# Optimization experiments

Hardware: AMD Instinct MI355X
Metric: run time of the kernel (lower is better)

Reference implementation:

```python
import jax, jax.numpy as jnp
import numpy as np


def setup_inputs() -> dict:
    key = jax.random.key(0)
    k1, k2, k3 = jax.random.split(key, 3)
    B, S, A, C = 128, 52, 5, 20
    predictions = jax.random.normal(k1, (B, A * (5 + C), S, S), dtype=jnp.float32)
    t = jax.random.uniform(k2, (B, S, S, A, 5 + C), dtype=jnp.float32)
    mask = (jax.random.uniform(k3, (B, S, S, A)) < 0.05).astype(jnp.float32)
    targets = t.at[..., 4].set(mask)
    anchors = jnp.array([[1.08, 1.19], [3.42, 4.41], [6.63, 11.38],
                         [9.42, 5.11], [16.62, 10.52]], dtype=jnp.float32)
    return {"predictions": predictions, "targets": targets, "anchors": anchors}


def _yolov2_loss(predictions, targets, anchors):
    B, pred_dim, S, _ = predictions.shape
    A = anchors.shape[0]
    C = pred_dim // A - 5
    # [B, A, 5+C, S, S] -> [B, S, S, A, 5+C]
    p = predictions.reshape(B, A, 5 + C, S, S).transpose(0, 3, 4, 1, 2)
    tx, ty, tw, th = p[..., 0], p[..., 1], p[..., 2], p[..., 3]
    conf_logits = p[..., 4]
    class_logits = p[..., 5:]

    gx, gy, gw, gh = targets[..., 0], targets[..., 1], targets[..., 2], targets[..., 3]
    obj_mask = targets[..., 4]
    class_target = targets[..., 5:]

    pred_cx = jax.nn.sigmoid(tx)
    pred_cy = jax.nn.sigmoid(ty)
    pred_w = jnp.exp(tw) * anchors[:, 0]  # broadcast over trailing A dim
    pred_h = jnp.exp(th) * anchors[:, 1]

    # grid offsets: dim 1 is i (row -> cy), dim 2 is j (col -> cx)
    jj = jnp.arange(S, dtype=jnp.float32)[None, None, :, None]
    ii = jnp.arange(S, dtype=jnp.float32)[None, :, None, None]
    cx_gt, cy_gt = gx + jj, gy + ii
    cx_pr, cy_pr = pred_cx + jj, pred_cy + ii

    # vectorized corner-form IoU (only used where obj_mask == 1)
    x1min, x1max = cx_gt - gw / 2, cx_gt + gw / 2
    y1min, y1max = cy_gt - gh / 2, cy_gt + gh / 2
    x2min, x2max = cx_pr - pred_w / 2, cx_pr + pred_w / 2
    y2min, y2max = cy_pr - pred_h / 2, cy_pr + pred_h / 2
    inter_w = jnp.clip(jnp.minimum(x1max, x2max) - jnp.maximum(x1min, x2min), 0.0)
    inter_h = jnp.clip(jnp.minimum(y1max, y2max) - jnp.maximum(y1min, y2min), 0.0)
    inter = inter_w * inter_h
    union = gw * gh + pred_w * pred_h - inter
    iou = jnp.where(union > 0, inter / union, 0.0)

    loss_xy = jnp.sum(obj_mask * (jnp.square(pred_cx - gx) + jnp.square(pred_cy - gy)))
    eps = 1e-6
    loss_wh = jnp.sum(obj_mask * (jnp.square(jnp.sqrt(pred_w + eps) - jnp.sqrt(gw + eps))
                                  + jnp.square(jnp.sqrt(pred_h + eps) - jnp.sqrt(gh + eps))))

    conf_pred = jax.nn.sigmoid(conf_logits)
    loss_obj = jnp.sum(obj_mask * jnp.square(iou - conf_pred))
    loss_noobj = jnp.sum((1.0 - obj_mask) * jnp.square(conf_pred))

    # BCE with logits: softplus(x) - x * t (stable via logaddexp)
    bce = jnp.logaddexp(0.0, class_logits) - class_logits * class_target
    loss_cls = jnp.sum(obj_mask[..., None] * bce)

    total = 5.0 * (loss_xy + loss_wh) + 5.0 * loss_obj + 0.5 * loss_noobj + loss_cls
    return total, loss_xy + loss_wh, loss_cls, loss_obj + loss_noobj


def reference(predictions, targets, anchors):
    # returns (total, coord, class, obj) matching the original dict values
    return _yolov2_loss(predictions, targets, anchors)
```

## Files before the change

kernel.cpp:

```cpp
#include <hip/hip_runtime.h>

#define S_DIM 52
#define SS 2704
#define NA 5
#define NC 20
#define NB 128
#define CELLS (NB * SS)
#define BLOCK 256
#define NBLK (CELLS / BLOCK)

__device__ __forceinline__ float fast_sigmoid(float x) {
    return __builtin_amdgcn_rcpf(1.0f + __expf(-x));
}
__device__ __forceinline__ float fast_softplus(float x) {
    return fmaxf(x, 0.0f) + __logf(1.0f + __expf(-fabsf(x)));
}

__device__ __forceinline__ bool block_reduce4(float v0, float v1, float v2, float v3,
                                              float a[4]) {
    #pragma unroll
    for (int off = 32; off > 0; off >>= 1) {
        v0 += __shfl_xor(v0, off, 64);
        v1 += __shfl_xor(v1, off, 64);
        v2 += __shfl_xor(v2, off, 64);
        v3 += __shfl_xor(v3, off, 64);
    }
    __shared__ float red[4][4];
    int wid = threadIdx.x >> 6, lane = threadIdx.x & 63;
    if (lane == 0) {
        red[wid][0] = v0; red[wid][1] = v1; red[wid][2] = v2; red[wid][3] = v3;
    }
    __syncthreads();
    if (threadIdx.x == 0) {
        #pragma unroll
        for (int q = 0; q < 4; ++q)
            a[q] = red[0][q] + red[1][q] + red[2][q] + red[3][q];
        return true;
    }
    return false;
}

__global__ __launch_bounds__(BLOCK) void yolo_main(
        const float* __restrict__ P,
        const float* __restrict__ T,
        const float* __restrict__ anch,
        float* __restrict__ partial) {
    int cell = blockIdx.x * BLOCK + threadIdx.x;
    int b  = cell / SS;
    int ij = cell - b * SS;
    const float* Pb = P + (size_t)b * 125 * SS + ij;
    const float* Tc = T + (size_t)cell * 125;

    float fl[NA], cf[NA];
    #pragma unroll
    for (int a = 0; a < NA; ++a) fl[a] = Tc[a * 25 + 4];
    #pragma unroll
    for (int a = 0; a < NA; ++a) cf[a] = Pb[(size_t)(a * 25 + 4) * SS];

    float s_xywh = 0.0f, s_cls = 0.0f, s_obj = 0.0f, s_noobj = 0.0f;

    #pragma unroll
    for (int a = 0; a < NA; ++a) {
        float cp = fast_sigmoid(cf[a]);
        if (fl[a] != 0.0f) {
            const float* Pa = Pb + (size_t)(a * 25) * SS;
            const float* Ta = Tc + a * 25;
            float aw = anch[2 * a], ahv = anch[2 * a + 1];

            float tx = Pa[0], ty = Pa[SS], tw = Pa[2 * SS], th = Pa[3 * SS];
            float gx = Ta[0], gy = Ta[1], gw = Ta[2], gh = Ta[3];
            float cx = fast_sigmoid(tx), cy = fast_sigmoid(ty);
            float pw = __expf(tw) * aw;
            float ph = __expf(th) * ahv;
            float iw = fmaxf(fminf(gx + 0.5f * gw, cx + 0.5f * pw) -
                             fmaxf(gx - 0.5f * gw, cx - 0.5f * pw), 0.0f);
            float ih = fmaxf(fminf(gy + 0.5f * gh, cy + 0.5f * ph) -
                             fmaxf(gy - 0.5f * gh, cy - 0.5f * ph), 0.0f);
            float inter = iw * ih;
            float uni   = gw * gh + pw * ph - inter;
            float iou   = (uni > 0.0f) ? inter * __builtin_amdgcn_rcpf(uni) : 0.0f;

            float dx = cx - gx, dy = cy - gy;
            s_xywh += dx * dx + dy * dy;
            const float eps = 1e-6f;
            float dw = __fsqrt_rn(pw + eps) - __fsqrt_rn(gw + eps);
            float dh = __fsqrt_rn(ph + eps) - __fsqrt_rn(gh + eps);
            s_xywh += dw * dw + dh * dh;

            float dob = iou - cp;
            s_obj += dob * dob;

            #pragma unroll
            for (int k = 0; k < NC; ++k) {
                float l = Pa[(size_t)(5 + k) * SS];
                float t = Ta[5 + k];
                s_cls += fast_softplus(l) - l * t;
            }
        } else {
            s_noobj += cp * cp;
        }
    }

    float a4[4];
    if (block_reduce4(s_xywh, s_cls, s_obj, s_noobj, a4)) {
        float* p = partial + (size_t)blockIdx.x * 4;
        p[0] = a4[0]; p[1] = a4[1]; p[2] = a4[2]; p[3] = a4[3];
    }
}

__global__ __launch_bounds__(BLOCK) void yolo_reduce(
        const float* __restrict__ partial, int n, float* __restrict__ out) {
    float v0 = 0.0f, v1 = 0.0f, v2 = 0.0f, v3 = 0.0f;
    for (int i = threadIdx.x; i < n; i += BLOCK) {
        const float* p = partial + (size_t)i * 4;
        v0 += p[0]; v1 += p[1]; v2 += p[2]; v3 += p[3];
    }
    float a4[4];
    if (block_reduce4(v0, v1, v2, v3, a4)) {
        float xywh = a4[0], cls = a4[1], obj = a4[2], noobj = a4[3];
        out[0] = 5.0f * xywh + 5.0f * obj + 0.5f * noobj + cls;
        out[1] = xywh;
        out[2] = cls;
        out[3] = obj + noobj;
    }
}

extern "C" void kernel_launch(void* const* d_in, const int* in_sizes, int n_in,
                              void* d_out, int out_size, void* d_ws, size_t ws_size,
                              hipStream_t stream) {
    const float* P = (const float*)d_in[0];
    const float* T = (const float*)d_in[1];
    const float* anch = (const float*)d_in[2];
    float* out = (float*)d_out;
    float* partial = (float*)d_ws;

    yolo_main<<<NBLK, BLOCK, 0, stream>>>(P, T, anch, partial);
    yolo_reduce<<<1, BLOCK, 0, stream>>>(partial, NBLK, out);
}
```

Measured before the change: 68.98 us.

## Stage target tile in LDS with coalesced float4 loads, one wave per anchor

Each block now handles 64 cells and copies their contiguous target rows (64×125 floats) into shared memory with coalesced float4 loads. Before, each thread read its own 125-float strided row. Each of the five waves then handles one anchor, so the per-anchor branch becomes per-thread rather than a loop inside each thread. The aim is to cut uncoalesced global reads of the target tensor. The cost is about 32KB of LDS per block, which may limit occupancy, plus an extra barrier. It also changes the number of partials sent to the reduce kernel.

```diff
diff --git a/kernel.cpp b/kernel.cpp
--- a/kernel.cpp
+++ b/kernel.cpp
@@ -1,13 +1,16 @@
 #include <hip/hip_runtime.h>
 
-#define S_DIM 52
 #define SS 2704
 #define NA 5
 #define NC 20
 #define NB 128
 #define CELLS (NB * SS)
-#define BLOCK 256
-#define NBLK (CELLS / BLOCK)
+#define TILE 64
+#define TPB 320
+#define NTILE (CELLS / TILE)
+#define TILE_F (TILE * 125)
+#define TILE_V4 (TILE_F / 4)
+#define RBLOCK 256
 
 __device__ __forceinline__ float fast_sigmoid(float x) {
     return __builtin_amdgcn_rcpf(1.0f + __expf(-x));
@@ -16,8 +19,104 @@
     return fmaxf(x, 0.0f) + __logf(1.0f + __expf(-fabsf(x)));
 }
 
-__device__ __forceinline__ bool block_reduce4(float v0, float v1, float v2, float v3,
-                                              float a[4]) {
+__global__ __launch_bounds__(TPB) void yolo_main(
+        const float* __restrict__ P,
+        const float* __restrict__ T,
+        const float* __restrict__ anch,
+        float* __restrict__ partial) {
+    __shared__ float lds[TILE_F];
+    __shared__ float red[NA][4];
+
+    int tile = blockIdx.x;
+
+    const float4* src = (const float4*)(T + (size_t)tile * TILE_F);
+    float4* dst = (float4*)lds;
+    #pragma unroll
+    for (int i = 0; i < 7; ++i) {
+        int idx = threadIdx.x + i * TPB;
+        if (idx < TILE_V4) dst[idx] = src[idx];
+    }
+    __syncthreads();
+
+    int a    = threadIdx.x >> 6;
+    int lane = threadIdx.x & 63;
+    int cell = tile * TILE + lane;
+    int b    = cell / SS;
+    int ij   = cell - b * SS;
+
+    const float* Pa = P + ((size_t)b * 125 + a * 25) * SS + ij;
+    const float* Tl = lds + lane * 125 + a * 25;
+    float aw  = anch[2 * a];
+    float ahv = anch[2 * a + 1];
+
+    float fl = Tl[4];
+    float cp = fast_sigmoid(Pa[4 * SS]);
+
+    float s_xywh = 0.0f, s_cls = 0.0f, s_obj = 0.0f, s_noobj = 0.0f;
+
+    if (fl != 0.0f) {
+        float tx = Pa[0], ty = Pa[SS], tw = Pa[2 * SS], th = Pa[3 * SS];
+        float gx = Tl[0], gy = Tl[1], gw = Tl[2], gh = Tl[3];
+        float cx = fast_sigmoid(tx), cy = fast_sigmoid(ty);
+        float pw = __expf(tw) * aw;
+        float ph = __expf(th) * ahv;
+        float iw = fmaxf(fminf(gx + 0.5f * gw, cx + 0.5f * pw) -
+                         fmaxf(gx - 0.5f * gw, cx - 0.5f * pw), 0.0f);
+        float ih = fmaxf(fminf(gy + 0.5f * gh, cy + 0.5f * ph) -
+                         fmaxf(gy - 0.5f * gh, cy - 0.5f * ph), 0.0f);
+        float inter = iw * ih;
+        float uni   = gw * gh + pw * ph - inter;
+        float iou   = (uni > 0.0f) ? inter * __builtin_amdgcn_rcpf(uni) : 0.0f;
+
+        float dx = cx - gx, dy = cy - gy;
+        s_xywh += dx * dx + dy * dy;
+        const float eps = 1e-6f;
+        float dw = __fsqrt_rn(pw + eps) - __fsqrt_rn(gw + eps);
+        float dh = __fsqrt_rn(ph + eps) - __fsqrt_rn(gh + eps);
+        s_xywh += dw * dw + dh * dh;
+
+        float dob = iou - cp;
+        s_obj += dob * dob;
+
+        #pragma unroll
+        for (int k = 0; k < NC; ++k) {
+            float l = Pa[(size_t)(5 + k) * SS];
+            float t = Tl[5 + k];
+            s_cls += fast_softplus(l) - l * t;
+        }
+    } else {
+        s_noobj = cp * cp;
+    }
+
+    #pragma unroll
+    for (int off = 32; off > 0; off >>= 1) {
+        s_xywh  += __shfl_xor(s_xywh,  off, 64);
+        s_cls   += __shfl_xor(s_cls,   off, 64);
+        s_obj   += __shfl_xor(s_obj,   off, 64);
+        s_noobj += __shfl_xor(s_noobj, off, 64);
+    }
+    if (lane == 0) {
+        red[a][0] = s_xywh; red[a][1] = s_cls; red[a][2] = s_obj; red[a][3] = s_noobj;
+    }
+    __syncthreads();
+    if (threadIdx.x == 0) {
+        float r0 = 0, r1 = 0, r2 = 0, r3 = 0;
+        #pragma unroll
+        for (int w = 0; w < NA; ++w) {
+            r0 += red[w][0]; r1 += red[w][1]; r2 += red[w][2]; r3 += red[w][3];
+        }
+        float* p = partial + (size_t)blockIdx.x * 4;
+        p[0] = r0; p[1] = r1; p[2] = r2; p[3] = r3;
+    }
+}
+
+__global__ __launch_bounds__(RBLOCK) void yolo_reduce(
+        const float* __restrict__ partial, int n, float* __restrict__ out) {
+    float v0 = 0.0f, v1 = 0.0f, v2 = 0.0f, v3 = 0.0f;
+    for (int i = threadIdx.x; i < n; i += RBLOCK) {
+        const float* p = partial + (size_t)i * 4;
+        v0 += p[0]; v1 += p[1]; v2 += p[2]; v3 += p[3];
+    }
     #pragma unroll
     for (int off = 32; off > 0; off >>= 1) {
         v0 += __shfl_xor(v0, off, 64);
@@ -32,92 +131,11 @@
     }
     __syncthreads();
     if (threadIdx.x == 0) {
+        float xywh = 0, cls = 0, obj = 0, noobj = 0;
         #pragma unroll
-        for (int q = 0; q < 4; ++q)
-            a[q] = red[0][q] + red[1][q] + red[2][q] + red[3][q];
-        return true;
-    }
-    return false;
-}
-
-__global__ __launch_bounds__(BLOCK) void yolo_main(
-        const float* __restrict__ P,
-        const float* __restrict__ T,
-        const float* __restrict__ anch,
-        float* __restrict__ partial) {
-    int cell = blockIdx.x * BLOCK + threadIdx.x;
-    int b  = cell / SS;
-    int ij = cell - b * SS;
-    const float* Pb = P + (size_t)b * 125 * SS + ij;
-    const float* Tc = T + (size_t)cell * 125;
-
-    float fl[NA], cf[NA];
-    #pragma unroll
-    for (int a = 0; a < NA; ++a) fl[a] = Tc[a * 25 + 4];
-    #pragma unroll
-    for (int a = 0; a < NA; ++a) cf[a] = Pb[(size_t)(a * 25 + 4) * SS];
-
-    float s_xywh = 0.0f, s_cls = 0.0f, s_obj = 0.0f, s_noobj = 0.0f;
-
-    #pragma unroll
-    for (int a = 0; a < NA; ++a) {
-        float cp = fast_sigmoid(cf[a]);
-        if (fl[a] != 0.0f) {
-            const float* Pa = Pb + (size_t)(a * 25) * SS;
-            const float* Ta = Tc + a * 25;
-            float aw = anch[2 * a], ahv = anch[2 * a + 1];
-
-            float tx = Pa[0], ty = Pa[SS], tw = Pa[2 * SS], th = Pa[3 * SS];
-            float gx = Ta[0], gy = Ta[1], gw = Ta[2], gh = Ta[3];
-            float cx = fast_sigmoid(tx), cy = fast_sigmoid(ty);
-            float pw = __expf(tw) * aw;
-            float ph = __expf(th) * ahv;
-            float iw = fmaxf(fminf(gx + 0.5f * gw, cx + 0.5f * pw) -
-                             fmaxf(gx - 0.5f * gw, cx - 0.5f * pw), 0.0f);
-            float ih = fmaxf(fminf(gy + 0.5f * gh, cy + 0.5f * ph) -
-                             fmaxf(gy - 0.5f * gh, cy - 0.5f * ph), 0.0f);
-            float inter = iw * ih;
-            float uni   = gw * gh + pw * ph - inter;
-            float iou   = (uni > 0.0f) ? inter * __builtin_amdgcn_rcpf(uni) : 0.0f;
-
-            float dx = cx - gx, dy = cy - gy;
-            s_xywh += dx * dx + dy * dy;
-            const float eps = 1e-6f;
-            float dw = __fsqrt_rn(pw + eps) - __fsqrt_rn(gw + eps);
-            float dh = __fsqrt_rn(ph + eps) - __fsqrt_rn(gh + eps);
-            s_xywh += dw * dw + dh * dh;
-
-            float dob = iou - cp;
-            s_obj += dob * dob;
-
-            #pragma unroll
-            for (int k = 0; k < NC; ++k) {
-                float l = Pa[(size_t)(5 + k) * SS];
-                float t = Ta[5 + k];
-                s_cls += fast_softplus(l) - l * t;
-            }
-        } else {
-            s_noobj += cp * cp;
+        for (int q = 0; q < 4; ++q) {
+            xywh += red[q][0]; cls += red[q][1]; obj += red[q][2]; noobj += red[q][3];
         }
-    }
-
-    float a4[4];
-    if (block_reduce4(s_xywh, s_cls, s_obj, s_noobj, a4)) {
-        float* p = partial + (size_t)blockIdx.x * 4;
-        p[0] = a4[0]; p[1] = a4[1]; p[2] = a4[2]; p[3] = a4[3];
-    }
-}
-
-__global__ __launch_bounds__(BLOCK) void yolo_reduce(
-        const float* __restrict__ partial, int n, float* __restrict__ out) {
-    float v0 = 0.0f, v1 = 0.0f, v2 = 0.0f, v3 = 0.0f;
-    for (int i = threadIdx.x; i < n; i += BLOCK) {
-        const float* p = partial + (size_t)i * 4;
-        v0 += p[0]; v1 += p[1]; v2 += p[2]; v3 += p[3];
-    }
-    float a4[4];
-    if (block_reduce4(v0, v1, v2, v3, a4)) {
-        float xywh = a4[0], cls = a4[1], obj = a4[2], noobj = a4[3];
         out[0] = 5.0f * xywh + 5.0f * obj + 0.5f * noobj + cls;
         out[1] = xywh;
         out[2] = cls;
@@ -134,6 +152,6 @@
     float* out = (float*)d_out;
     float* partial = (float*)d_ws;
 
-    yolo_main<<<NBLK, BLOCK, 0, stream>>>(P, T, anch, partial);
-    yolo_reduce<<<1, BLOCK, 0, stream>>>(partial, NBLK, out);
+    yolo_main<<<NTILE, TPB, 0, stream>>>(P, T, anch, partial);
+    yolo_reduce<<<1, RBLOCK, 0, stream>>>(partial, NTILE, out);
 }
```

New measurement: 65.58 us. -4.9%, faster.
